# Performance work log

Measured on AMD Instinct MI355X. Metric: run time of the kernel, lower is better.

The kernel has to match this reference:

```python
import jax, jax.numpy as jnp
import numpy as np

H = 512   # n_hidden
V = 32000 # n_words
T1 = 128  # encoder length
T2 = 64   # decoder length
B = 32    # batch


def _gru_cell(x, h, W_ih, W_hh, b_ih, b_hh):
    # PyTorch GRUCell math. x: [B, in], h: [B, H]
    gi = x @ W_ih.T + b_ih            # [B, 3H]
    gh = h @ W_hh.T + b_hh            # [B, 3H]
    i_r, i_z, i_n = jnp.split(gi, 3, axis=-1)
    h_r, h_z, h_n = jnp.split(gh, 3, axis=-1)
    r = jax.nn.sigmoid(i_r + h_r)
    z = jax.nn.sigmoid(i_z + h_z)
    n = jnp.tanh(i_n + r * h_n)
    return (1.0 - z) * n + z * h


def setup_inputs() -> dict:
    key = jax.random.key(0)
    ks = jax.random.split(key, 18)
    s = 0.05
    f32 = jnp.float32
    return {
        "decoder_inputs": jax.random.randint(ks[0], (T2, B), 0, V),
        "state": jax.random.normal(ks[1], (2, B, H), f32),
        "encoder_outputs": jax.random.normal(ks[2], (T1, B, H), f32),
        "emb": jax.random.normal(ks[3], (V, H), f32) * s,
        "wa_W": jax.random.normal(ks[4], (H, 2 * H), f32) * s,
        "wa_b": jax.random.normal(ks[5], (H,), f32) * s,
        "va_W": jax.random.normal(ks[6], (1, H), f32) * s,
        "W_ih0": jax.random.normal(ks[7], (3 * H, 2 * H), f32) * s,
        "W_hh0": jax.random.normal(ks[8], (3 * H, H), f32) * s,
        "b_ih0": jax.random.normal(ks[9], (3 * H,), f32) * s,
        "b_hh0": jax.random.normal(ks[10], (3 * H,), f32) * s,
        "W_ih1": jax.random.normal(ks[11], (3 * H, H), f32) * s,
        "W_hh1": jax.random.normal(ks[12], (3 * H, H), f32) * s,
        "b_ih1": jax.random.normal(ks[13], (3 * H,), f32) * s,
        "b_hh1": jax.random.normal(ks[14], (3 * H,), f32) * s,
        "out_W": jax.random.normal(ks[15], (V, H), f32) * s,
        "out_b": jax.random.normal(ks[16], (V,), f32) * s,
    }


def reference(decoder_inputs, state, encoder_outputs, emb, wa_W, wa_b, va_W,
              W_ih0, W_hh0, b_ih0, b_hh0, W_ih1, W_hh1, b_ih1, b_hh1,
              out_W, out_b):
    x = emb[decoder_inputs]                               # [T2, B, H]
    # wa(concat([xt_rep, enc])) == xt @ Wx.T + enc @ We.T + b  (split the weight)
    Wx = wa_W[:, :H]                                      # [H, H]
    We = wa_W[:, H:]                                      # [H, H]
    enc_proj = jnp.einsum('tbh,oh->tbo', encoder_outputs, We) + wa_b  # [T1,B,H]
    va = va_W[0]                                          # [H]

    def step(h, xt):  # h: [2,B,H], xt: [B,H]
        u = jnp.tanh(xt @ Wx.T + enc_proj)                # [T1, B, H]
        e = jnp.einsum('tbh,h->tb', u, va)                # [T1, B]
        score = jax.nn.softmax(e, axis=0)                 # softmax over T1
        att_v = jnp.einsum('tbh,tb->bh', encoder_outputs, score)  # [B, H]
        gin = jnp.concatenate([xt, att_v], axis=-1)       # [B, 2H]
        h0 = _gru_cell(gin, h[0], W_ih0, W_hh0, b_ih0, b_hh0)
        h1 = _gru_cell(h0, h[1], W_ih1, W_hh1, b_ih1, b_hh1)
        return jnp.stack([h0, h1]), (h1, score)

    h_final, (ys, scores) = jax.lax.scan(step, state, x)  # ys: [T2, B, H]
    y = jnp.einsum('tbh,vh->tbv', ys, out_W) + out_b      # [T2, B, V]
    last_score = scores[-1][:, :, None]                   # [T1, B, 1] (torch returns last-step score)
    return y, h_final, last_score
```

## Files before the change

### kernel.cpp

```cpp
#include <hip/hip_runtime.h>
#include <hip/hip_bf16.h>
#include <stdint.h>

#define HH   512
#define VV   32000
#define T1N  128
#define T2N  64
#define BB   32

typedef __attribute__((ext_vector_type(8))) short short8;
typedef __attribute__((ext_vector_type(4))) float f32x4;

__device__ __forceinline__ ushort f2b(float f) {
  unsigned u = __float_as_uint(f);
  unsigned r = (u + 0x7fffu + ((u >> 16) & 1u)) >> 16;
  return (ushort)r;
}
__device__ __forceinline__ float blo(unsigned u){ return __uint_as_float(u << 16); }
__device__ __forceinline__ float bhi(unsigned u){ return __uint_as_float(u & 0xffff0000u); }

__device__ __forceinline__ float fast_tanh(float x) {
  float ax = fabsf(x);
  float e  = __expf(-2.f * ax);
  float t  = (1.f - e) / (1.f + e);
  return x < 0.f ? -t : t;
}
__device__ __forceinline__ float fsig(float x) { return 1.f / (1.f + __expf(-x)); }

__global__ __launch_bounds__(256) void k_cvt(const float* __restrict__ s, ushort* __restrict__ d, int n) {
  int i = (blockIdx.x * 256 + threadIdx.x) * 4;
  if (i < n) {
    float4 v = *(const float4*)(s + i);
    ushort4 o = { f2b(v.x), f2b(v.y), f2b(v.z), f2b(v.w) };
    *(ushort4*)(d + i) = o;
  }
}

__global__ __launch_bounds__(256) void k_cvt_wa(const float* __restrict__ wa,
                                                ushort* __restrict__ Wx, ushort* __restrict__ We) {
  int i = (blockIdx.x * 256 + threadIdx.x) * 4;
  int half = (i >= HH * HH);
  int j = i & (HH * HH - 1);
  int o = j >> 9, c = j & 511;
  const float* s = wa + (size_t)o * 1024 + c + (half ? 512 : 0);
  float4 v = *(const float4*)s;
  ushort4 ov = { f2b(v.x), f2b(v.y), f2b(v.z), f2b(v.w) };
  *(ushort4*)((half ? We : Wx) + j) = ov;
}

__global__ __launch_bounds__(256) void k_embed(const int* __restrict__ toks, const float* __restrict__ emb,
                                               ushort* __restrict__ ginB) {
  int i = (blockIdx.x * 256 + threadIdx.x) * 4;
  int row = i >> 9, c = i & 511;
  int tok = toks[row];
  float4 v = *(const float4*)(emb + (size_t)tok * HH + c);
  ushort4 ov = { f2b(v.x), f2b(v.y), f2b(v.z), f2b(v.w) };
  *(ushort4*)(ginB + (size_t)row * 1024 + c) = ov;
}

__global__ __launch_bounds__(256) void k_gemm(const ushort* __restrict__ A, int lda,
                                              const ushort* __restrict__ B,
                                              const float* __restrict__ bias,
                                              float* __restrict__ C, int ldc, int K) {
  __shared__ ushort sA[128 * 32];
  __shared__ ushort sB[128 * 32];
  const int tid  = threadIdx.x;
  const int bm   = blockIdx.y * 128;
  const int bn   = blockIdx.x * 128;
  const int lane = tid & 63;
  const int wave = tid >> 6;
  const int wm   = (wave >> 1) * 64;
  const int wn   = (wave & 1) * 64;
  const int m16  = lane & 15;
  const int quad = lane >> 4;

  f32x4 acc[4][4] = {};

  for (int k0 = 0; k0 < K; k0 += 32) {
#pragma unroll
    for (int q = 0; q < 2; ++q) {
      int idx = q * 256 + tid;
      int row = idx >> 2;
      int kc  = (idx & 3) << 3;
      uint4 va = *(const uint4*)(A + (size_t)(bm + row) * lda + k0 + kc);
      *(uint4*)(&sA[idx * 8]) = va;
      uint4 vb = *(const uint4*)(B + (size_t)(bn + row) * K + k0 + kc);
      *(uint4*)(&sB[idx * 8]) = vb;
    }
    __syncthreads();
    short8 a[4], b[4];
#pragma unroll
    for (int i = 0; i < 4; ++i)
      a[i] = *(const short8*)(&sA[(wm + i * 16 + m16) * 32 + quad * 8]);
#pragma unroll
    for (int j = 0; j < 4; ++j)
      b[j] = *(const short8*)(&sB[(wn + j * 16 + m16) * 32 + quad * 8]);
#pragma unroll
    for (int i = 0; i < 4; ++i)
#pragma unroll
      for (int j = 0; j < 4; ++j)
        acc[i][j] = __builtin_amdgcn_mfma_f32_16x16x32_bf16(a[i], b[j], acc[i][j], 0, 0, 0);
    __syncthreads();
  }
#pragma unroll
  for (int i = 0; i < 4; ++i) {
    int gm = bm + wm + i * 16 + quad * 4;
#pragma unroll
    for (int j = 0; j < 4; ++j) {
      int gn = bn + wn + j * 16 + m16;
      float bv = bias ? bias[gn] : 0.f;
#pragma unroll
      for (int r = 0; r < 4; ++r)
        C[(size_t)(gm + r) * ldc + gn] = acc[i][j][r] + bv;
    }
  }
}

__global__ __launch_bounds__(256) void k_gemm_b16(const ushort* __restrict__ A, int lda,
                                                  const ushort* __restrict__ B,
                                                  const float* __restrict__ bias,
                                                  ushort* __restrict__ C, int ldc, int K) {
  __shared__ ushort sA[128 * 32];
  __shared__ ushort sB[128 * 32];
  const int tid  = threadIdx.x;
  const int bm   = blockIdx.y * 128;
  const int bn   = blockIdx.x * 128;
  const int lane = tid & 63;
  const int wave = tid >> 6;
  const int wm   = (wave >> 1) * 64;
  const int wn   = (wave & 1) * 64;
  const int m16  = lane & 15;
  const int quad = lane >> 4;

  f32x4 acc[4][4] = {};

  for (int k0 = 0; k0 < K; k0 += 32) {
#pragma unroll
    for (int q = 0; q < 2; ++q) {
      int idx = q * 256 + tid;
      int row = idx >> 2;
      int kc  = (idx & 3) << 3;
      uint4 va = *(const uint4*)(A + (size_t)(bm + row) * lda + k0 + kc);
      *(uint4*)(&sA[idx * 8]) = va;
      uint4 vb = *(const uint4*)(B + (size_t)(bn + row) * K + k0 + kc);
      *(uint4*)(&sB[idx * 8]) = vb;
    }
    __syncthreads();
    short8 a[4], b[4];
#pragma unroll
    for (int i = 0; i < 4; ++i)
      a[i] = *(const short8*)(&sA[(wm + i * 16 + m16) * 32 + quad * 8]);
#pragma unroll
    for (int j = 0; j < 4; ++j)
      b[j] = *(const short8*)(&sB[(wn + j * 16 + m16) * 32 + quad * 8]);
#pragma unroll
    for (int i = 0; i < 4; ++i)
#pragma unroll
      for (int j = 0; j < 4; ++j)
        acc[i][j] = __builtin_amdgcn_mfma_f32_16x16x32_bf16(a[i], b[j], acc[i][j], 0, 0, 0);
    __syncthreads();
  }
#pragma unroll
  for (int i = 0; i < 4; ++i) {
    int gm = bm + wm + i * 16 + quad * 4;
#pragma unroll
    for (int j = 0; j < 4; ++j) {
      int gn = bn + wn + j * 16 + m16;
      float bv = bias ? bias[gn] : 0.f;
#pragma unroll
      for (int r = 0; r < 4; ++r)
        C[(size_t)(gm + r) * ldc + gn] = f2b(acc[i][j][r] + bv);
    }
  }
}

__global__ __launch_bounds__(256) void k_scores(const float* __restrict__ xproj,
                                                const float* __restrict__ encp,
                                                const float* __restrict__ vaW,
                                                float* __restrict__ e) {
  int t2g = blockIdx.x >> 5;
  int b   = blockIdx.x & 31;
  __shared__ float sx[4][512];
  int tid = threadIdx.x;
  for (int i = tid; i < 4 * 512; i += 256) {
    int tt = i >> 9, h = i & 511;
    sx[tt][h] = xproj[((size_t)(t2g * 4 + tt) * BB + b) * HH + h];
  }
  __syncthreads();
  int lane = tid & 63, w = tid >> 6;
  int h8 = lane * 8;
  float va[8];
#pragma unroll
  for (int j = 0; j < 8; ++j) va[j] = vaW[h8 + j];
  for (int t1 = w; t1 < T1N; t1 += 4) {
    const float* ep = encp + ((size_t)t1 * BB + b) * HH + h8;
    float ev[8];
    *(float4*)&ev[0] = *(const float4*)ep;
    *(float4*)&ev[4] = *(const float4*)(ep + 4);
    float s0 = 0, s1 = 0, s2 = 0, s3 = 0;
#pragma unroll
    for (int j = 0; j < 8; ++j) {
      float epj = ev[j], vj = va[j];
      s0 += fast_tanh(sx[0][h8 + j] + epj) * vj;
      s1 += fast_tanh(sx[1][h8 + j] + epj) * vj;
      s2 += fast_tanh(sx[2][h8 + j] + epj) * vj;
      s3 += fast_tanh(sx[3][h8 + j] + epj) * vj;
    }
#pragma unroll
    for (int off = 32; off; off >>= 1) {
      s0 += __shfl_down(s0, off);
      s1 += __shfl_down(s1, off);
      s2 += __shfl_down(s2, off);
      s3 += __shfl_down(s3, off);
    }
    if (lane == 0) {
      size_t base = ((size_t)(t2g * 4) * BB + b) * T1N + t1;
      e[base]                 = s0;
      e[base + 1 * BB * T1N]  = s1;
      e[base + 2 * BB * T1N]  = s2;
      e[base + 3 * BB * T1N]  = s3;
    }
  }
}

__global__ __launch_bounds__(128) void k_softmax(const float* __restrict__ e, float* __restrict__ score,
                                                 float* __restrict__ out_last) {
  int row = blockIdx.x;
  int tid = threadIdx.x;
  float v = e[(size_t)row * T1N + tid];
  __shared__ float red[128];
  red[tid] = v; __syncthreads();
  for (int s = 64; s; s >>= 1) { if (tid < s) red[tid] = fmaxf(red[tid], red[tid + s]); __syncthreads(); }
  float mx = red[0]; __syncthreads();
  float p = __expf(v - mx);
  red[tid] = p; __syncthreads();
  for (int s = 64; s; s >>= 1) { if (tid < s) red[tid] += red[tid + s]; __syncthreads(); }
  float sc = p / red[0];
  score[(size_t)row * T1N + tid] = sc;
  if ((row >> 5) == T2N - 1) out_last[tid * BB + (row & 31)] = sc;
}

__global__ __launch_bounds__(256) void k_attv(const float* __restrict__ enc, const float* __restrict__ score,
                                              ushort* __restrict__ ginB) {
  int t2g = blockIdx.x >> 5;
  int b   = blockIdx.x & 31;
  __shared__ float ssc[8][T1N];
  int tid = threadIdx.x;
  for (int i = tid; i < 8 * T1N; i += 256) {
    int j = i >> 7, t1 = i & 127;
    ssc[j][t1] = score[((size_t)(t2g * 8 + j) * BB + b) * T1N + t1];
  }
  __syncthreads();
  float a0[8] = {}, a1[8] = {};
  for (int t1 = 0; t1 < T1N; ++t1) {
    const float* er = enc + ((size_t)t1 * BB + b) * HH;
    float e0 = er[tid], e1 = er[tid + 256];
#pragma unroll
    for (int j = 0; j < 8; ++j) { a0[j] += e0 * ssc[j][t1]; a1[j] += e1 * ssc[j][t1]; }
  }
#pragma unroll
  for (int j = 0; j < 8; ++j) {
    size_t r = (size_t)(t2g * 8 + j) * BB + b;
    ginB[r * 1024 + 512 + tid]       = f2b(a0[j]);
    ginB[r * 1024 + 512 + tid + 256] = f2b(a1[j]);
  }
}

__device__ __forceinline__ void gru_pair(uint gr, uint gz, uint gn, uint hr, uint hz, uint hn,
                                         float hold0, float hold1, float& o0, float& o1) {
  float r0 = fsig(blo(gr) + blo(hr));
  float r1 = fsig(bhi(gr) + bhi(hr));
  float z0 = fsig(blo(gz) + blo(hz));
  float z1 = fsig(bhi(gz) + bhi(hz));
  float n0 = fast_tanh(blo(gn) + r0 * blo(hn));
  float n1 = fast_tanh(bhi(gn) + r1 * bhi(hn));
  o0 = (1.f - z0) * n0 + z0 * hold0;
  o1 = (1.f - z1) * n1 + z1 * hold1;
}

__device__ __forceinline__ void gbar(unsigned* bar, unsigned nblk) {
  __syncthreads();
  if (threadIdx.x == 0) {
    unsigned g = __hip_atomic_load(bar + 16, __ATOMIC_RELAXED, __HIP_MEMORY_SCOPE_AGENT);
    unsigned old = __hip_atomic_fetch_add(bar, 1u, __ATOMIC_ACQ_REL, __HIP_MEMORY_SCOPE_AGENT);
    if (old == nblk - 1u) {
      __hip_atomic_store(bar, 0u, __ATOMIC_RELAXED, __HIP_MEMORY_SCOPE_AGENT);
      __hip_atomic_store(bar + 16, g + 1u, __ATOMIC_RELEASE, __HIP_MEMORY_SCOPE_AGENT);
    } else {
      while (__hip_atomic_load(bar + 16, __ATOMIC_ACQUIRE, __HIP_MEMORY_SCOPE_AGENT) == g)
        __builtin_amdgcn_s_sleep(2);
    }
  }
  __syncthreads();
}

__global__ void k_bar_init(unsigned* bar) { bar[0] = 0u; bar[16] = 0u; }

struct RecurP {
  const ushort* Whh0B; const ushort* Whh1B; const ushort* Wih1B;
  const float* bhh0; const float* bhh1; const float* bih1;
  const ushort* gi0B;
  const float* state;
  const ushort* stateB;
  ushort* gh0x;
  ushort* gh1b0; ushort* gh1b1;
  ushort* gi1x;
  float* h0b0; float* h0b1;
  float* h1b0; float* h1b1;
  ushort* h0B0; ushort* h0B1;
  float* h_out;
  ushort* ysB;
  unsigned* bar;
};

__global__ __launch_bounds__(256, 1) void k_recur(RecurP p) {
  __shared__ ushort sH[32 * 520];
  __shared__ ushort sW0[32 * 520];
  __shared__ ushort sW1[32 * 520];
  __shared__ ushort sWi[32 * 520];
  const int tid  = threadIdx.x;
  const int blk  = blockIdx.x;
  const int lane = tid & 63, wave = tid >> 6;
  const int bt = wave & 1, nt = wave >> 1;
  const int m16 = lane & 15, quad = lane >> 4;
  const int nrow = blk * 32 + nt * 16 + m16;
  const int k0 = tid * 2;
  const unsigned nblk = gridDim.x;
  const float* state1 = p.state + BB * HH;

  const float bv0 = p.bhh0[nrow];
  const float bv1 = p.bhh1[nrow];
  const float bvi = p.bih1[nrow];
  const int brow = bt * 16 + quad * 4;

  for (int i = tid * 4; i < 32 * 512; i += 256 * 4) {
    int row = i >> 9, col = i & 511;
    size_t g = (size_t)(blk * 32 + row) * 512 + col;
    *(uint2*)(&sW0[row * 520 + col]) = *(const uint2*)(p.Whh0B + g);
    *(uint2*)(&sW1[row * 520 + col]) = *(const uint2*)(p.Whh1B + g);
    *(uint2*)(&sWi[row * 520 + col]) = *(const uint2*)(p.Wih1B + g);
  }

#pragma unroll 1
  for (int t = 0; t < T2N; ++t) {
    const int par = t & 1;
    if (t == 0) {
      for (int i = tid; i < 16384; i += 256) {
        int b = i >> 9, k = i & 511;
        sH[b * 520 + k] = f2b(state1[i]);
      }
    } else {
      const ushort* gh1in = par ? p.gh1b0 : p.gh1b1;
      const float*  h1in  = (t <= 1) ? state1 : (par ? p.h1b1 : p.h1b0);
      float*        h1out = par ? p.h1b0 : p.h1b1;
      ushort*       ysprev = p.ysB + (size_t)(t - 1) * BB * HH;
#pragma unroll 4
      for (int b = 0; b < 32; ++b) {
        const ushort* gi = p.gi1x + b * 1536 + k0;
        const ushort* gh = gh1in + b * 1536 + k0;
        uint gir = *(const uint*)(gi);
        uint giz = *(const uint*)(gi + 512);
        uint gin = *(const uint*)(gi + 1024);
        uint hr  = *(const uint*)(gh);
        uint hz  = *(const uint*)(gh + 512);
        uint hn  = *(const uint*)(gh + 1024);
        float2 hold = *(const float2*)(h1in + b * 512 + k0);
        float o0, o1;
        gru_pair(gir, giz, gin, hr, hz, hn, hold.x, hold.y, o0, o1);
        uint hb = (uint)f2b(o0) | ((uint)f2b(o1) << 16);
        *(uint*)(&sH[b * 520 + k0]) = hb;
        if (blk == b) {
          *(float2*)(h1out + b * 512 + k0) = make_float2(o0, o1);
          *(uint*)(ysprev + b * 512 + k0) = hb;
        }
      }
    }
    __syncthreads();

    {
      const ushort* h0Bin = (t == 0) ? p.stateB : (par ? p.h0B0 : p.h0B1);
      ushort* gh1out = par ? p.gh1b1 : p.gh1b0;
      f32x4 acc0 = {0.f, 0.f, 0.f, 0.f}, acc1 = {0.f, 0.f, 0.f, 0.f};
      const ushort* Arow0  = h0Bin + (bt * 16 + m16) * 512 + quad * 8;
      const ushort* Brow0  = &sW0[(nt * 16 + m16) * 520 + quad * 8];
      const ushort* Brow1  = &sW1[(nt * 16 + m16) * 520 + quad * 8];
      const ushort* sArow1 = &sH[(bt * 16 + m16) * 520 + quad * 8];
#pragma unroll 4
      for (int kc = 0; kc < 16; ++kc) {
        short8 a0 = *(const short8*)(Arow0 + kc * 32);
        short8 b0 = *(const short8*)(Brow0 + kc * 32);
        acc0 = __builtin_amdgcn_mfma_f32_16x16x32_bf16(a0, b0, acc0, 0, 0, 0);
        short8 a1 = *(const short8*)(sArow1 + kc * 32);
        short8 b1 = *(const short8*)(Brow1 + kc * 32);
        acc1 = __builtin_amdgcn_mfma_f32_16x16x32_bf16(a1, b1, acc1, 0, 0, 0);
      }
#pragma unroll
      for (int r = 0; r < 4; ++r) {
        p.gh0x[(brow + r) * 1536 + nrow] = f2b(acc0[r] + bv0);
        gh1out[(brow + r) * 1536 + nrow] = f2b(acc1[r] + bv1);
      }
    }
    gbar(p.bar, nblk);

    {
      const ushort* gi0t  = p.gi0B + (size_t)t * 32 * 1536;
      const float*  h0in  = (t == 0) ? p.state : (par ? p.h0b0 : p.h0b1);
      float*        h0out = par ? p.h0b1 : p.h0b0;
      ushort*       h0Bout = par ? p.h0B1 : p.h0B0;
#pragma unroll 4
      for (int b = 0; b < 32; ++b) {
        const ushort* gi = gi0t + b * 1536 + k0;
        const ushort* gh = p.gh0x + b * 1536 + k0;
        uint gir = *(const uint*)(gi);
        uint giz = *(const uint*)(gi + 512);
        uint gin = *(const uint*)(gi + 1024);
        uint hr  = *(const uint*)(gh);
        uint hz  = *(const uint*)(gh + 512);
        uint hn  = *(const uint*)(gh + 1024);
        float2 hold = *(const float2*)(h0in + b * 512 + k0);
        float o0, o1;
        gru_pair(gir, giz, gin, hr, hz, hn, hold.x, hold.y, o0, o1);
        uint hb = (uint)f2b(o0) | ((uint)f2b(o1) << 16);
        *(uint*)(&sH[b * 520 + k0]) = hb;
        if (blk == b) {
          *(float2*)(h0out + b * 512 + k0) = make_float2(o0, o1);
          *(uint*)(h0Bout + b * 512 + k0) = hb;
        }
      }
      __syncthreads();

      f32x4 acc = {0.f, 0.f, 0.f, 0.f};
      const ushort* Brow  = &sWi[(nt * 16 + m16) * 520 + quad * 8];
      const ushort* sArow = &sH[(bt * 16 + m16) * 520 + quad * 8];
#pragma unroll 4
      for (int kc = 0; kc < 16; ++kc) {
        short8 a = *(const short8*)(sArow + kc * 32);
        short8 b = *(const short8*)(Brow + kc * 32);
        acc = __builtin_amdgcn_mfma_f32_16x16x32_bf16(a, b, acc, 0, 0, 0);
      }
#pragma unroll
      for (int r = 0; r < 4; ++r)
        p.gi1x[(brow + r) * 1536 + nrow] = f2b(acc[r] + bvi);
    }
    gbar(p.bar, nblk);
  }

  if (blk < 32) {
    const int b = blk;
    const ushort* gi = p.gi1x + b * 1536 + k0;
    const ushort* gh = p.gh1b1 + b * 1536 + k0;
    uint gir = *(const uint*)(gi);
    uint giz = *(const uint*)(gi + 512);
    uint gin = *(const uint*)(gi + 1024);
    uint hr  = *(const uint*)(gh);
    uint hz  = *(const uint*)(gh + 512);
    uint hn  = *(const uint*)(gh + 1024);
    float2 hold = *(const float2*)(p.h1b0 + b * 512 + k0);
    float o0, o1;
    gru_pair(gir, giz, gin, hr, hz, hn, hold.x, hold.y, o0, o1);
    *(uint*)(p.ysB + (size_t)63 * BB * HH + b * 512 + k0) = (uint)f2b(o0) | ((uint)f2b(o1) << 16);
    p.h_out[16384 + b * 512 + k0]     = o0;
    p.h_out[16384 + b * 512 + k0 + 1] = o1;
    float2 h0p = *(const float2*)(p.h0b1 + b * 512 + k0);
    *(float2*)(p.h_out + b * 512 + k0) = h0p;
  }
}

extern "C" void kernel_launch(void* const* d_in, const int* in_sizes, int n_in,
                              void* d_out, int out_size, void* d_ws, size_t ws_size,
                              hipStream_t stream) {
  const int*   toks  = (const int*)d_in[0];
  const float* state = (const float*)d_in[1];
  const float* enc   = (const float*)d_in[2];
  const float* emb   = (const float*)d_in[3];
  const float* wa_W  = (const float*)d_in[4];
  const float* wa_b  = (const float*)d_in[5];
  const float* va    = (const float*)d_in[6];
  const float* b_ih0 = (const float*)d_in[9];
  const float* b_hh0 = (const float*)d_in[10];
  const float* b_ih1 = (const float*)d_in[13];
  const float* b_hh1 = (const float*)d_in[14];
  const float* out_W = (const float*)d_in[15];
  const float* out_b = (const float*)d_in[16];
  const float* W_ih0 = (const float*)d_in[7];
  const float* W_hh0 = (const float*)d_in[8];
  const float* W_ih1 = (const float*)d_in[11];
  const float* W_hh1 = (const float*)d_in[12];

  float* y_out  = (float*)d_out;
  float* h_out  = y_out + (size_t)T2N * BB * VV;
  float* ls_out = h_out + 2 * BB * HH;

  char* ws = (char*)d_ws;
  size_t off = 0;
  auto alloc = [&](size_t bytes) -> void* {
    void* p = ws + off;
    off += (bytes + 255) & ~(size_t)255;
    return p;
  };
  ushort* encB   = (ushort*)alloc((size_t)T1N * BB * HH * 2);
  ushort* ginB   = (ushort*)alloc((size_t)T2N * BB * 2 * HH * 2);
  ushort* WeB    = (ushort*)alloc((size_t)HH * HH * 2);
  ushort* WxB    = (ushort*)alloc((size_t)HH * HH * 2);
  ushort* Wih0B  = (ushort*)alloc((size_t)3 * HH * 2 * HH * 2);
  ushort* Whh0B  = (ushort*)alloc((size_t)3 * HH * HH * 2);
  ushort* Wih1B  = (ushort*)alloc((size_t)3 * HH * HH * 2);
  ushort* Whh1B  = (ushort*)alloc((size_t)3 * HH * HH * 2);
  ushort* outWB  = (ushort*)alloc((size_t)VV * HH * 2);
  ushort* stateB = (ushort*)alloc((size_t)BB * HH * 2);
  float* encproj = (float*)alloc((size_t)T1N * BB * HH * 4);
  float* xproj   = (float*)alloc((size_t)T2N * BB * HH * 4);
  float* eM      = (float*)alloc((size_t)T2N * BB * T1N * 4);
  float* score   = (float*)alloc((size_t)T2N * BB * T1N * 4);
  ushort* gi0B   = (ushort*)alloc((size_t)T2N * BB * 3 * HH * 2);
  ushort* gh0x   = (ushort*)alloc((size_t)BB * 3 * HH * 2);
  ushort* gh1buf0 = (ushort*)alloc((size_t)BB * 3 * HH * 2);
  ushort* gh1buf1 = (ushort*)alloc((size_t)BB * 3 * HH * 2);
  ushort* gi1x   = (ushort*)alloc((size_t)BB * 3 * HH * 2);
  float* h0buf0  = (float*)alloc((size_t)BB * HH * 4);
  float* h0buf1  = (float*)alloc((size_t)BB * HH * 4);
  float* h1buf0  = (float*)alloc((size_t)BB * HH * 4);
  float* h1buf1  = (float*)alloc((size_t)BB * HH * 4);
  ushort* h0bufB0 = (ushort*)alloc((size_t)BB * HH * 2);
  ushort* h0bufB1 = (ushort*)alloc((size_t)BB * HH * 2);
  ushort* ysB    = (ushort*)alloc((size_t)T2N * BB * HH * 2);
  unsigned* bar  = (unsigned*)alloc(256);

  k_bar_init<<<1, 1, 0, stream>>>(bar);
  k_cvt<<<VV * HH / 1024, 256, 0, stream>>>(out_W, outWB, VV * HH);
  k_cvt<<<T1N * BB * HH / 1024, 256, 0, stream>>>(enc, encB, T1N * BB * HH);
  k_cvt<<<3 * HH * 2 * HH / 1024, 256, 0, stream>>>(W_ih0, Wih0B, 3 * HH * 2 * HH);
  k_cvt<<<3 * HH * HH / 1024, 256, 0, stream>>>(W_hh0, Whh0B, 3 * HH * HH);
  k_cvt<<<3 * HH * HH / 1024, 256, 0, stream>>>(W_ih1, Wih1B, 3 * HH * HH);
  k_cvt<<<3 * HH * HH / 1024, 256, 0, stream>>>(W_hh1, Whh1B, 3 * HH * HH);
  k_cvt<<<BB * HH / 1024, 256, 0, stream>>>(state, stateB, BB * HH);
  k_cvt_wa<<<2 * HH * HH / 1024, 256, 0, stream>>>(wa_W, WxB, WeB);
  k_embed<<<T2N * BB * HH / 1024, 256, 0, stream>>>(toks, emb, ginB);

  k_gemm<<<dim3(HH / 128, T1N * BB / 128), 256, 0, stream>>>(encB, HH, WeB, wa_b, encproj, HH, HH);
  k_gemm<<<dim3(HH / 128, T2N * BB / 128), 256, 0, stream>>>(ginB, 2 * HH, WxB, nullptr, xproj, HH, HH);

  k_scores<<<512, 256, 0, stream>>>(xproj, encproj, va, eM);
  k_softmax<<<T2N * BB, 128, 0, stream>>>(eM, score, ls_out);
  k_attv<<<256, 256, 0, stream>>>(enc, score, ginB);

  k_gemm_b16<<<dim3(3 * HH / 128, T2N * BB / 128), 256, 0, stream>>>(ginB, 2 * HH, Wih0B, b_ih0, gi0B, 3 * HH, 2 * HH);

  RecurP rp;
  rp.Whh0B = Whh0B; rp.Whh1B = Whh1B; rp.Wih1B = Wih1B;
  rp.bhh0 = b_hh0; rp.bhh1 = b_hh1; rp.bih1 = b_ih1;
  rp.gi0B = gi0B;
  rp.state = state; rp.stateB = stateB;
  rp.gh0x = gh0x;
  rp.gh1b0 = gh1buf0; rp.gh1b1 = gh1buf1;
  rp.gi1x = gi1x;
  rp.h0b0 = h0buf0; rp.h0b1 = h0buf1;
  rp.h1b0 = h1buf0; rp.h1b1 = h1buf1;
  rp.h0B0 = h0bufB0; rp.h0B1 = h0bufB1;
  rp.h_out = h_out; rp.ysB = ysB;
  rp.bar = bar;
  void* kargs[] = { &rp };
  hipLaunchCooperativeKernel((const void*)k_recur, dim3(48), dim3(256), kargs, 0, stream);

  k_gemm<<<dim3(VV / 128, T2N * BB / 128), 256, 0, stream>>>(ysB, HH, outWB, out_b, y_out, VV, HH);
}
```

Baseline: 3.798 ms.

## Replace flat grid barrier with hierarchical per-XCD barrier in recurrence kernel

The single-counter grid barrier used twice per timestep in the persistent GRU recurrence kernel is replaced with a two-level scheme. Each block reads its XCC_ID, one leader per XCD is elected, and leaders wait on a global arrival counter, sync among themselves, then release a per-XCD flag. Non-leader blocks spin on that local flag and invalidate their cache. The goal is to cut cross-die atomic contention and barrier latency on the 128 barriers, at the cost of added complexity, a timeout-based spin that could silently break correctness, and reliance on the XCC_ID hardware register.

```diff
diff --git a/kernel.cpp b/kernel.cpp
--- a/kernel.cpp
+++ b/kernel.cpp
@@ -278,23 +278,42 @@
   o1 = (1.f - z1) * n1 + z1 * hold1;
 }
 
-__device__ __forceinline__ void gbar(unsigned* bar, unsigned nblk) {
+__device__ __forceinline__ unsigned armw(unsigned* p, unsigned v) {
+  return __hip_atomic_fetch_add(p, v, __ATOMIC_RELAXED, __HIP_MEMORY_SCOPE_AGENT);
+}
+
+#define SPIN_GE(addr, target)                                             \
+  {                                                                       \
+    unsigned long long _t0 = __builtin_amdgcn_s_memrealtime();            \
+    while (armw((addr), 0u) < (target)) {                                 \
+      __builtin_amdgcn_s_sleep(1);                                        \
+      if (__builtin_amdgcn_s_memrealtime() - _t0 > 5000000ull) break;     \
+    }                                                                     \
+  }
+
+__device__ __forceinline__ void gbarH(unsigned* bs, int myxcd, bool leader,
+                                      unsigned nblk, unsigned nxcd, unsigned ep) {
   __syncthreads();
   if (threadIdx.x == 0) {
-    unsigned g = __hip_atomic_load(bar + 16, __ATOMIC_RELAXED, __HIP_MEMORY_SCOPE_AGENT);
-    unsigned old = __hip_atomic_fetch_add(bar, 1u, __ATOMIC_ACQ_REL, __HIP_MEMORY_SCOPE_AGENT);
-    if (old == nblk - 1u) {
-      __hip_atomic_store(bar, 0u, __ATOMIC_RELAXED, __HIP_MEMORY_SCOPE_AGENT);
-      __hip_atomic_store(bar + 16, g + 1u, __ATOMIC_RELEASE, __HIP_MEMORY_SCOPE_AGENT);
+    armw(bs + 144, 1u);
+    if (leader) {
+      SPIN_GE(bs + 144, nblk * ep);
+      __builtin_amdgcn_fence(__ATOMIC_RELEASE, "agent");
+      armw(bs + 160, 1u);
+      SPIN_GE(bs + 160, nxcd * ep);
+      __builtin_amdgcn_fence(__ATOMIC_ACQUIRE, "agent");
+      armw(bs + 176 + myxcd * 16, 1u);
     } else {
-      while (__hip_atomic_load(bar + 16, __ATOMIC_ACQUIRE, __HIP_MEMORY_SCOPE_AGENT) == g)
-        __builtin_amdgcn_s_sleep(2);
+      SPIN_GE(bs + 176 + myxcd * 16, ep);
+      asm volatile("s_waitcnt vmcnt(0)\n\tbuffer_inv sc0" ::: "memory");
     }
   }
   __syncthreads();
 }
 
-__global__ void k_bar_init(unsigned* bar) { bar[0] = 0u; bar[16] = 0u; }
+__global__ void k_bar_init(unsigned* bs) {
+  for (int i = threadIdx.x; i < 512; i += 256) bs[i] = 0u;
+}
 
 struct RecurP {
   const ushort* Whh0B; const ushort* Whh1B; const ushort* Wih1B;
@@ -327,6 +346,24 @@
   const int k0 = tid * 2;
   const unsigned nblk = gridDim.x;
   const float* state1 = p.state + BB * HH;
+  unsigned* bs = p.bar;
+
+  unsigned xcc;
+  asm volatile("s_getreg_b32 %0, hwreg(HW_REG_XCC_ID)" : "=s"(xcc));
+  xcc &= 7u;
+  __shared__ int s_xcd, s_leader, s_nxcd;
+  if (tid == 0) {
+    unsigned rank = armw(bs + xcc * 16, 1u);
+    armw(bs + 128, 1u);
+    SPIN_GE(bs + 128, nblk);
+    unsigned nx = 0;
+    for (int i = 0; i < 8; ++i) nx += (armw(bs + i * 16, 0u) > 0u) ? 1u : 0u;
+    s_xcd = (int)xcc; s_leader = (rank == 0u) ? 1 : 0; s_nxcd = (int)nx;
+  }
+  __syncthreads();
+  const int myxcd = s_xcd;
+  const bool leader = (s_leader != 0);
+  const unsigned nxcd = (unsigned)s_nxcd;
 
   const float bv0 = p.bhh0[nrow];
   const float bv1 = p.bhh1[nrow];
@@ -400,7 +437,7 @@
         gh1out[(brow + r) * 1536 + nrow] = f2b(acc1[r] + bv1);
       }
     }
-    gbar(p.bar, nblk);
+    gbarH(bs, myxcd, leader, nblk, nxcd, (unsigned)(2 * t + 1));
 
     {
       const ushort* gi0t  = p.gi0B + (size_t)t * 32 * 1536;
@@ -442,7 +479,7 @@
       for (int r = 0; r < 4; ++r)
         p.gi1x[(brow + r) * 1536 + nrow] = f2b(acc[r] + bvi);
     }
-    gbar(p.bar, nblk);
+    gbarH(bs, myxcd, leader, nblk, nxcd, (unsigned)(2 * t + 2));
   }
 
   if (blk < 32) {
@@ -524,9 +561,9 @@
   ushort* h0bufB0 = (ushort*)alloc((size_t)BB * HH * 2);
   ushort* h0bufB1 = (ushort*)alloc((size_t)BB * HH * 2);
   ushort* ysB    = (ushort*)alloc((size_t)T2N * BB * HH * 2);
-  unsigned* bar  = (unsigned*)alloc(256);
-
-  k_bar_init<<<1, 1, 0, stream>>>(bar);
+  unsigned* bar  = (unsigned*)alloc(2048);
+
+  k_bar_init<<<1, 256, 0, stream>>>(bar);
   k_cvt<<<VV * HH / 1024, 256, 0, stream>>>(out_W, outWB, VV * HH);
   k_cvt<<<T1N * BB * HH / 1024, 256, 0, stream>>>(enc, encB, T1N * BB * HH);
   k_cvt<<<3 * HH * 2 * HH / 1024, 256, 0, stream>>>(W_ih0, Wih0B, 3 * HH * 2 * HH);
```

After: 3.631 ms. -4.4%, faster.
